# Kernel optimization log

Measured on AMD Instinct MI355X. Metric: run time of the kernel, lower is better.

## Reference

```python
import jax, jax.numpy as jnp
import numpy as np
import math

D_K = 64

def setup_inputs() -> dict:
    key = jax.random.key(0)
    kq, kk, kv, km = jax.random.split(key, 4)
    B, H, S, D = 2, 16, 2048, D_K
    Q = jax.random.normal(kq, (B, H, S, D), dtype=jnp.float32)
    K = jax.random.normal(kk, (B, H, S, D), dtype=jnp.float32)
    V = jax.random.normal(kv, (B, H, S, D), dtype=jnp.float32)
    attn_mask = jax.random.randint(km, (B, 1, S, S), 0, 2, dtype=jnp.int32)
    return {"Q": Q, "K": K, "V": V, "attn_mask": attn_mask}

def reference(Q, K, V, attn_mask):
    # scores: [B, H, S, S]
    scores = jnp.einsum('bhqd,bhkd->bhqk', Q, K) / math.sqrt(D_K)
    scores = jnp.where(attn_mask == 0, jnp.float32(-1e9), scores)
    attn = jax.nn.softmax(scores, axis=-1)
    context = jnp.einsum('bhqk,bhkd->bhqd', attn, V)
    return (context, attn)
```

## Files before the change

kernel.cpp:

```cpp
#include <hip/hip_runtime.h>
#include <math.h>

#define B_   2
#define H_   16
#define S_   2048
#define D_   64
#define QT   16
#define NQT  (S_/QT)
#define NBLK (B_*H_*NQT)

typedef __attribute__((ext_vector_type(8))) short  bf16x8;
typedef __attribute__((ext_vector_type(8))) unsigned short u16x8;
typedef __attribute__((ext_vector_type(4))) float  f32x4;

static __device__ __forceinline__ short f2bf(float f) {
    union { float f; unsigned u; } x; x.f = f;
    unsigned r = x.u + 0x7fffu + ((x.u >> 16) & 1u);
    return (short)(r >> 16);
}
static __device__ __forceinline__ float bf2f(unsigned short u) {
    union { unsigned u; float f; } x; x.u = ((unsigned)u) << 16;
    return x.f;
}

__global__ __launch_bounds__(256, 2)
void sdpa_mfma_kernel(const float* __restrict__ Q, const float* __restrict__ K,
                      const float* __restrict__ V, const int* __restrict__ M,
                      float* __restrict__ ctx_out, float* __restrict__ attn_out) {
    __shared__ __align__(16) unsigned short sc[QT][S_];
    __shared__ float linv[QT];

    const int t  = threadIdx.x;
    const int w  = t >> 6;
    const int l  = t & 63;
    const int lr = l & 15;
    const int lg = l >> 4;

    const int orig = blockIdx.x;
    const int swz  = (orig & 7) * (NBLK / 8) + (orig >> 3);
    const int bh   = swz >> 7;
    const int qt   = swz & 127;
    const int b    = bh >> 4;
    const int q0   = qt * QT;

    const float* Qb = Q + (size_t)bh * S_ * D_;
    const float* Kb = K + (size_t)bh * S_ * D_;
    const float* Vb = V + (size_t)bh * S_ * D_;
    const int*   Mb = M + (size_t)b * S_ * S_;

    bf16x8 aq0, aq1;
    {
        const float* qp = Qb + (size_t)(q0 + lr) * D_ + lg * 8;
        #pragma unroll
        for (int j = 0; j < 8; ++j) aq0[j] = f2bf(0.125f * qp[j]);
        #pragma unroll
        for (int j = 0; j < 8; ++j) aq1[j] = f2bf(0.125f * qp[32 + j]);
    }

    #pragma unroll 2
    for (int kt = 0; kt < 32; ++kt) {
        const int k0 = w * 512 + kt * 16;
        const float* kp = Kb + (size_t)(k0 + lr) * D_ + lg * 8;
        bf16x8 bk0, bk1;
        #pragma unroll
        for (int j = 0; j < 8; ++j) bk0[j] = f2bf(kp[j]);
        #pragma unroll
        for (int j = 0; j < 8; ++j) bk1[j] = f2bf(kp[32 + j]);
        f32x4 c = {0.f, 0.f, 0.f, 0.f};
        c = __builtin_amdgcn_mfma_f32_16x16x32_bf16(aq0, bk0, c, 0, 0, 0);
        c = __builtin_amdgcn_mfma_f32_16x16x32_bf16(aq1, bk1, c, 0, 0, 0);
        const int key = k0 + lr;
        #pragma unroll
        for (int r = 0; r < 4; ++r) {
            const int row = lg * 4 + r;
            const int mk  = Mb[(size_t)(q0 + row) * S_ + key];
            const float s = mk ? c[r] : -1e9f;
            sc[row][(((key >> 3) ^ (row & 7)) << 3) + (key & 7)] = (unsigned short)f2bf(s);
        }
    }
    __syncthreads();

    #pragma unroll
    for (int r = 0; r < 4; ++r) {
        const int q = w * 4 + r;
        const int x = q & 7;
        float f[32];
        #pragma unroll
        for (int i = 0; i < 4; ++i) {
            const u16x8 u = *(const u16x8*)&sc[q][(i * 64 + l) * 8];
            #pragma unroll
            for (int j = 0; j < 8; ++j) f[i * 8 + j] = bf2f(u[j]);
        }
        float m = f[0];
        #pragma unroll
        for (int j = 1; j < 32; ++j) m = fmaxf(m, f[j]);
        #pragma unroll
        for (int off = 32; off; off >>= 1) m = fmaxf(m, __shfl_xor(m, off));
        float ssum = 0.f;
        #pragma unroll
        for (int j = 0; j < 32; ++j) { f[j] = __expf(f[j] - m); ssum += f[j]; }
        #pragma unroll
        for (int off = 32; off; off >>= 1) ssum += __shfl_xor(ssum, off);
        const float il = 1.0f / ssum;
        if (l == 0) linv[q] = il;

        float* arow = attn_out + ((size_t)bh * S_ + q0 + q) * S_;
        #pragma unroll
        for (int i = 0; i < 4; ++i) {
            const int us = i * 64 + l;
            u16x8 ub;
            #pragma unroll
            for (int j = 0; j < 8; ++j) ub[j] = (unsigned short)f2bf(f[i * 8 + j]);
            *(u16x8*)&sc[q][us * 8] = ub;
            const int uk = us ^ x;
            float4 o0, o1;
            o0.x = f[i*8+0]*il; o0.y = f[i*8+1]*il; o0.z = f[i*8+2]*il; o0.w = f[i*8+3]*il;
            o1.x = f[i*8+4]*il; o1.y = f[i*8+5]*il; o1.z = f[i*8+6]*il; o1.w = f[i*8+7]*il;
            *(float4*)(arow + (size_t)uk * 8)     = o0;
            *(float4*)(arow + (size_t)uk * 8 + 4) = o1;
        }
    }
    __syncthreads();

    {
        const int d0 = w * 16;
        f32x4 cc = {0.f, 0.f, 0.f, 0.f};
        #pragma unroll 2
        for (int ks = 0; ks < 64; ++ks) {
            const int k0 = ks * 32;
            const int un = ((k0 >> 3) + lg) ^ (lr & 7);
            const bf16x8 pa = *(const bf16x8*)&sc[lr][un * 8];
            const float* vp = Vb + (size_t)(k0 + lg * 8) * D_ + d0 + lr;
            bf16x8 vb;
            #pragma unroll
            for (int j = 0; j < 8; ++j) vb[j] = f2bf(vp[(size_t)j * D_]);
            cc = __builtin_amdgcn_mfma_f32_16x16x32_bf16(pa, vb, cc, 0, 0, 0);
        }
        #pragma unroll
        for (int r = 0; r < 4; ++r) {
            const int q = lg * 4 + r;
            ctx_out[((size_t)bh * S_ + q0 + q) * D_ + d0 + lr] = cc[r] * linv[q];
        }
    }
}

extern "C" void kernel_launch(void* const* d_in, const int* in_sizes, int n_in,
                              void* d_out, int out_size, void* d_ws, size_t ws_size,
                              hipStream_t stream) {
    const float* Q = (const float*)d_in[0];
    const float* K = (const float*)d_in[1];
    const float* V = (const float*)d_in[2];
    const int*   M = (const int*)d_in[3];

    float* ctx  = (float*)d_out;
    float* attn = (float*)d_out + (size_t)B_ * H_ * S_ * D_;

    sdpa_mfma_kernel<<<dim3(NBLK), dim3(256), 0, stream>>>(Q, K, V, M, ctx, attn);
}
```

Before: 457.0 us.

## Precompute bf16 K, transposed bf16 V and packed mask bits in prep kernels

Adds three preprocessing kernels that convert K to bf16, transpose and convert V to bf16, and pack the int32 mask into 64-bit ballot bitmasks, all stored in workspace. The main kernel, templated on PREP, then issues vector loads of bf16 operands and reads mask bits from shared memory. Each block no longer reloads and converts fp32 K/V and the int32 mask, which the 128 query tiles per head previously repeated many times. The cost is three extra launches and workspace traffic, and the fallback path runs only when the workspace is too small.

```diff
diff --git a/kernel.cpp b/kernel.cpp
--- a/kernel.cpp
+++ b/kernel.cpp
@@ -23,11 +23,51 @@
     return x.f;
 }
 
+__global__ __launch_bounds__(256) void cvtK_kernel(const float* __restrict__ K,
+                                                   unsigned short* __restrict__ Kb) {
+    const size_t i = ((size_t)blockIdx.x * 256 + threadIdx.x) * 8;
+    const float4 a = *(const float4*)(K + i);
+    const float4 b = *(const float4*)(K + i + 4);
+    u16x8 o;
+    o[0]=f2bf(a.x); o[1]=f2bf(a.y); o[2]=f2bf(a.z); o[3]=f2bf(a.w);
+    o[4]=f2bf(b.x); o[5]=f2bf(b.y); o[6]=f2bf(b.z); o[7]=f2bf(b.w);
+    *(u16x8*)(Kb + i) = o;
+}
+
+__global__ __launch_bounds__(256) void cvtVT_kernel(const float* __restrict__ V,
+                                                    unsigned short* __restrict__ Vt) {
+    const int l  = threadIdx.x & 63;
+    const int w  = threadIdx.x >> 6;
+    const int bh = blockIdx.x >> 6;
+    const int kc = (blockIdx.x & 63) * 32 + w * 8;
+    const float* vp = V + ((size_t)bh * S_ + kc) * D_ + l;
+    u16x8 o;
+    #pragma unroll
+    for (int j = 0; j < 8; ++j) o[j] = f2bf(vp[(size_t)j * D_]);
+    *(u16x8*)(Vt + ((size_t)bh * D_ + l) * S_ + kc) = o;
+}
+
+__global__ __launch_bounds__(256) void maskbits_kernel(const int* __restrict__ M,
+                                                       unsigned long long* __restrict__ bits) {
+    const int w = threadIdx.x >> 6, l = threadIdx.x & 63;
+    const size_t wl0 = (size_t)(blockIdx.x * 4 + w) * 32;
+    for (int it = 0; it < 32; ++it) {
+        const int mk = M[(wl0 + it) * 64 + l];
+        const unsigned long long bm = __ballot(mk != 0);
+        if (l == 0) bits[wl0 + it] = bm;
+    }
+}
+
+template<int PREP>
 __global__ __launch_bounds__(256, 2)
 void sdpa_mfma_kernel(const float* __restrict__ Q, const float* __restrict__ K,
                       const float* __restrict__ V, const int* __restrict__ M,
+                      const unsigned short* __restrict__ Kb,
+                      const unsigned short* __restrict__ Vt,
+                      const unsigned* __restrict__ bits,
                       float* __restrict__ ctx_out, float* __restrict__ attn_out) {
     __shared__ __align__(16) unsigned short sc[QT][S_];
+    __shared__ __align__(16) unsigned mb[QT][64];
     __shared__ float linv[QT];
 
     const int t  = threadIdx.x;
@@ -44,9 +84,12 @@
     const int q0   = qt * QT;
 
     const float* Qb = Q + (size_t)bh * S_ * D_;
-    const float* Kb = K + (size_t)bh * S_ * D_;
-    const float* Vb = V + (size_t)bh * S_ * D_;
     const int*   Mb = M + (size_t)b * S_ * S_;
+
+    if (PREP) {
+        const int r = t >> 4, cw = (t & 15) * 4;
+        *(uint4*)&mb[r][cw] = *(const uint4*)(bits + ((size_t)b * S_ + q0 + r) * 64 + cw);
+    }
 
     bf16x8 aq0, aq1;
     {
@@ -56,16 +99,23 @@
         #pragma unroll
         for (int j = 0; j < 8; ++j) aq1[j] = f2bf(0.125f * qp[32 + j]);
     }
+    if (PREP) __syncthreads();
 
     #pragma unroll 2
     for (int kt = 0; kt < 32; ++kt) {
         const int k0 = w * 512 + kt * 16;
-        const float* kp = Kb + (size_t)(k0 + lr) * D_ + lg * 8;
         bf16x8 bk0, bk1;
-        #pragma unroll
-        for (int j = 0; j < 8; ++j) bk0[j] = f2bf(kp[j]);
-        #pragma unroll
-        for (int j = 0; j < 8; ++j) bk1[j] = f2bf(kp[32 + j]);
+        if (PREP) {
+            const unsigned short* kp = Kb + ((size_t)bh * S_ + k0 + lr) * D_ + lg * 8;
+            bk0 = *(const bf16x8*)kp;
+            bk1 = *(const bf16x8*)(kp + 32);
+        } else {
+            const float* kp = K + ((size_t)bh * S_ + k0 + lr) * D_ + lg * 8;
+            #pragma unroll
+            for (int j = 0; j < 8; ++j) bk0[j] = f2bf(kp[j]);
+            #pragma unroll
+            for (int j = 0; j < 8; ++j) bk1[j] = f2bf(kp[32 + j]);
+        }
         f32x4 c = {0.f, 0.f, 0.f, 0.f};
         c = __builtin_amdgcn_mfma_f32_16x16x32_bf16(aq0, bk0, c, 0, 0, 0);
         c = __builtin_amdgcn_mfma_f32_16x16x32_bf16(aq1, bk1, c, 0, 0, 0);
@@ -73,7 +123,9 @@
         #pragma unroll
         for (int r = 0; r < 4; ++r) {
             const int row = lg * 4 + r;
-            const int mk  = Mb[(size_t)(q0 + row) * S_ + key];
+            int mk;
+            if (PREP) mk = (mb[row][key >> 5] >> (key & 31)) & 1;
+            else      mk = Mb[(size_t)(q0 + row) * S_ + key];
             const float s = mk ? c[r] : -1e9f;
             sc[row][(((key >> 3) ^ (row & 7)) << 3) + (key & 7)] = (unsigned short)f2bf(s);
         }
@@ -130,10 +182,14 @@
             const int k0 = ks * 32;
             const int un = ((k0 >> 3) + lg) ^ (lr & 7);
             const bf16x8 pa = *(const bf16x8*)&sc[lr][un * 8];
-            const float* vp = Vb + (size_t)(k0 + lg * 8) * D_ + d0 + lr;
             bf16x8 vb;
-            #pragma unroll
-            for (int j = 0; j < 8; ++j) vb[j] = f2bf(vp[(size_t)j * D_]);
+            if (PREP) {
+                vb = *(const bf16x8*)(Vt + ((size_t)bh * D_ + d0 + lr) * S_ + k0 + lg * 8);
+            } else {
+                const float* vp = V + ((size_t)bh * S_ + k0 + lg * 8) * D_ + d0 + lr;
+                #pragma unroll
+                for (int j = 0; j < 8; ++j) vb[j] = f2bf(vp[(size_t)j * D_]);
+            }
             cc = __builtin_amdgcn_mfma_f32_16x16x32_bf16(pa, vb, cc, 0, 0, 0);
         }
         #pragma unroll
@@ -155,5 +211,21 @@
     float* ctx  = (float*)d_out;
     float* attn = (float*)d_out + (size_t)B_ * H_ * S_ * D_;
 
-    sdpa_mfma_kernel<<<dim3(NBLK), dim3(256), 0, stream>>>(Q, K, V, M, ctx, attn);
-}
+    const size_t nEl      = (size_t)B_ * H_ * S_ * D_;
+    const size_t nBits64  = (size_t)B_ * S_ * (S_ / 64);
+    const size_t need     = nEl * 2 * 2 + nBits64 * 8;
+
+    if (ws_size >= need) {
+        unsigned short* Kb = (unsigned short*)d_ws;
+        unsigned short* Vt = Kb + nEl;
+        unsigned long long* bits = (unsigned long long*)(Vt + nEl);
+        cvtK_kernel    <<<dim3((int)(nEl / 2048)), dim3(256), 0, stream>>>(K, Kb);
+        cvtVT_kernel   <<<dim3(B_ * H_ * (S_ / 32)), dim3(256), 0, stream>>>(V, Vt);
+        maskbits_kernel<<<dim3((int)(nBits64 / 128)), dim3(256), 0, stream>>>(M, bits);
+        sdpa_mfma_kernel<1><<<dim3(NBLK), dim3(256), 0, stream>>>(
+            Q, K, V, M, Kb, Vt, (const unsigned*)bits, ctx, attn);
+    } else {
+        sdpa_mfma_kernel<0><<<dim3(NBLK), dim3(256), 0, stream>>>(
+            Q, K, V, M, nullptr, nullptr, nullptr, ctx, attn);
+    }
+}
```

Result: faster. 374.9 us (-18.0%).
